# Performance work log

Measured on AMD Instinct MI355X. Metric: run time of the kernel, lower is better.

## Reference

```python
import jax, jax.numpy as jnp
import numpy as np

TRAIN_ROIS = 200
POS_RATIO = 0.33
POS_MAX = int(TRAIN_ROIS * POS_RATIO)  # 66
BBOX_STD = np.array([0.1, 0.1, 0.2, 0.2], dtype=np.float32)


def _iou(boxes1, boxes2):
    # boxes1 [N,4], boxes2 [G,4] in (y1,x1,y2,x2) -> IoU [N,G]
    b1 = boxes1[:, None, :]
    b2 = boxes2[None, :, :]
    y1 = jnp.maximum(b1[..., 0], b2[..., 0])
    x1 = jnp.maximum(b1[..., 1], b2[..., 1])
    y2 = jnp.minimum(b1[..., 2], b2[..., 2])
    x2 = jnp.minimum(b1[..., 3], b2[..., 3])
    inter = jnp.maximum(x2 - x1, 0.0) * jnp.maximum(y2 - y1, 0.0)
    a1 = (b1[..., 2] - b1[..., 0]) * (b1[..., 3] - b1[..., 1])
    a2 = (b2[..., 2] - b2[..., 0]) * (b2[..., 3] - b2[..., 1])
    union = a1 + a2 - inter
    return inter / jnp.where(union > 0, union, 1.0)


def _box_refine(box, gt):
    # standard Mask R-CNN box_refinement_graph
    h = box[..., 2] - box[..., 0]
    w = box[..., 3] - box[..., 1]
    cy = box[..., 0] + 0.5 * h
    cx = box[..., 1] + 0.5 * w
    gh = gt[..., 2] - gt[..., 0]
    gw = gt[..., 3] - gt[..., 1]
    gcy = gt[..., 0] + 0.5 * gh
    gcx = gt[..., 1] + 0.5 * gw
    return jnp.stack([(gcy - cy) / h, (gcx - cx) / w,
                      jnp.log(gh / h), jnp.log(gw / w)], axis=-1)


def _per_image(proposals, gt_boxes, gt_captions, scores):
    T = TRAIN_ROIS
    valid_p = jnp.sum(jnp.abs(proposals), axis=1) > 0   # trim_zeros on proposals
    valid_g = jnp.sum(jnp.abs(gt_boxes), axis=1) > 0    # trim_zeros on gt
    # IoU only feeds comparisons/argmax (pure index selection) -> no grad path
    overlaps = jax.lax.stop_gradient(_iou(proposals, gt_boxes))
    overlaps = jnp.where(valid_g[None, :], overlaps, -1.0)
    roi_iou_max = jnp.max(overlaps, axis=1)
    pos_bool = valid_p & (roi_iou_max >= 0.5)
    neg_bool = valid_p & (roi_iou_max < 0.5)
    # deterministic stand-in for tf.random.shuffle[:count]: first `count` in index order
    pos_idx = jnp.where(pos_bool, size=POS_MAX, fill_value=0)[0]
    pos_cnt = jnp.minimum(jnp.sum(pos_bool), POS_MAX)
    pos_valid = jnp.arange(POS_MAX) < pos_cnt
    neg_target = (pos_cnt.astype(jnp.float32) / POS_RATIO).astype(jnp.int32) - pos_cnt
    neg_idx = jnp.where(neg_bool, size=T, fill_value=0)[0]
    neg_cnt = jnp.minimum(jnp.minimum(neg_target, jnp.sum(neg_bool)), T - pos_cnt)
    neg_valid = jnp.arange(T) < neg_cnt

    positive_rois = proposals[pos_idx]                  # [POS_MAX,4]
    negative_rois = proposals[neg_idx]                  # [T,4]
    gt_assign = jnp.argmax(overlaps[pos_idx], axis=1)   # [POS_MAX]
    roi_gt_boxes = gt_boxes[gt_assign]
    roi_gt_captions = gt_captions[gt_assign]
    roi_gt_scores = scores[gt_assign]
    # for padded (invalid) positive slots, use the roi itself -> zero, finite deltas
    safe_gt = jnp.where(pos_valid[:, None], roi_gt_boxes, positive_rois)
    deltas = _box_refine(positive_rois, safe_gt) / jnp.asarray(BBOX_STD)

    # positives occupy slots [0,pos_cnt), negatives [pos_cnt, pos_cnt+neg_cnt), rest zero-padded
    pos_slots = jnp.where(pos_valid, jnp.arange(POS_MAX), T)   # T is out-of-range -> dropped
    neg_slots = jnp.where(neg_valid, pos_cnt + jnp.arange(T), T)
    rois = (jnp.zeros((T, 4), proposals.dtype)
            .at[pos_slots].set(positive_rois, mode='drop')
            .at[neg_slots].set(negative_rois, mode='drop'))
    out_deltas = jnp.zeros((T, 4), proposals.dtype).at[pos_slots].set(deltas, mode='drop')
    out_caps = jnp.zeros((T, gt_captions.shape[1]), gt_captions.dtype).at[pos_slots].set(roi_gt_captions, mode='drop')
    out_scores = jnp.zeros((T,), scores.dtype).at[pos_slots].set(roi_gt_scores, mode='drop')
    return rois, out_deltas, out_caps, out_scores


def setup_inputs() -> dict:
    key = jax.random.key(0)
    B, N, G = 8, 4096, 512
    k1, k2, k3, k4, k5 = jax.random.split(key, 5)
    c = jax.random.uniform(k1, (B, N, 2))                   # box centers (y,x)
    s = jax.random.uniform(k2, (B, N, 2)) * 0.2 + 0.02      # box sizes
    lo = jnp.clip(c - 0.5 * s, 0.0, 1.0)
    hi = jnp.clip(c + 0.5 * s, 0.0, 1.0)
    proposals = jnp.concatenate([lo, hi], axis=-1)          # (y1,x1,y2,x2)
    # gt boxes = perturbed copies of first G proposals (ensures IoU>=0.5 positives exist)
    p = proposals[:, :G, :] + jax.random.normal(k3, (B, G, 4)) * 0.02
    y1 = jnp.minimum(p[..., 0], p[..., 2]); y2 = jnp.maximum(p[..., 0], p[..., 2]) + 1e-3
    x1 = jnp.minimum(p[..., 1], p[..., 3]); x2 = jnp.maximum(p[..., 1], p[..., 3]) + 1e-3
    gt_boxes = jnp.clip(jnp.stack([y1, x1, y2, x2], axis=-1), 0.0, 1.0)
    # exercise the zero-trim logic: zero-pad tails
    proposals = proposals.at[:, N - 256:, :].set(0.0)
    gt_boxes = gt_boxes.at[:, G - 32:, :].set(0.0)
    gt_captions = jax.random.randint(k4, (B, G, 15), 0, 10000, dtype=jnp.int32)
    scores = jax.random.uniform(k5, (B, G))
    return {"proposals": proposals, "gt_boxes": gt_boxes,
            "gt_captions": gt_captions, "scores": scores}


def reference(proposals, gt_boxes, gt_captions, scores):
    return jax.vmap(_per_image)(proposals, gt_boxes, gt_captions, scores)
```

## Files before the change

### kernel.cpp

```cpp
#include <hip/hip_runtime.h>
#include <math.h>

#define BB   8
#define NP   4096
#define NG   512
#define TT   200
#define PMAX 66

#define CH   8
#define PB   32
#define NBLK (NP / PB)

__global__ __launch_bounds__(256) void iou_phase(
    const float* __restrict__ proposals, const float* __restrict__ gt,
    int* __restrict__ argj, unsigned int* __restrict__ posmask,
    unsigned int* __restrict__ negmask) {
#pragma clang fp contract(off)
  const int b     = blockIdx.x >> 7;
  const int blk   = blockIdx.x & 127;
  const int pbase = blk * PB;

  __shared__ float4 sgt[NG];
  __shared__ float  sa2[NG];
  __shared__ short  sidx[NG];
  __shared__ int    s_nv;
  __shared__ float  rbest[CH][PB];
  __shared__ int    ridx[CH][PB];

  const int tid = threadIdx.x;

  if (tid < 64) {
    const float4* gtb4 = (const float4*)(gt + (size_t)b * NG * 4);
    int cnt = 0;
    for (int base = 0; base < NG; base += 64) {
      int j = base + tid;
      float4 g = gtb4[j];
      bool v = (fabsf(g.x) + fabsf(g.y) + fabsf(g.z) + fabsf(g.w)) > 0.0f;
      unsigned long long m = __ballot(v);
      if (v) {
        int k = cnt + __popcll(m & ((1ull << tid) - 1ull));
        sgt[k]  = g;
        sa2[k]  = (g.z - g.x) * (g.w - g.y);
        sidx[k] = (short)j;
      }
      cnt += __popcll(m);
    }
    if (tid == 0) s_nv = cnt;
  }
  __syncthreads();

  const int nv  = s_nv;
  const int csz = (nv + CH - 1) / CH;

  const int plocal  = tid & (PB - 1);
  const int chunkid = tid >> 5;
  const int i       = pbase + plocal;

  const float4 p = ((const float4*)proposals)[(size_t)b * NP + i];
  const float a1 = (p.z - p.x) * (p.w - p.y);

  int j0 = chunkid * csz;
  int j1 = j0 + csz; if (j1 > nv) j1 = nv;
  if (j0 > nv) j0 = nv;

  float best = -INFINITY;
  int bj = 0;
  for (int j = j0; j < j1; ++j) {
    float4 g = sgt[j];
    float y1 = fmaxf(p.x, g.x);
    float x1 = fmaxf(p.y, g.y);
    float y2 = fminf(p.z, g.z);
    float x2 = fminf(p.w, g.w);
    float inter = fmaxf(x2 - x1, 0.0f) * fmaxf(y2 - y1, 0.0f);
    float un = a1 + sa2[j] - inter;
    float iou = inter / (un > 0.0f ? un : 1.0f);
    if (iou > best) { best = iou; bj = (int)sidx[j]; }
  }
  rbest[chunkid][plocal] = best;
  ridx[chunkid][plocal]  = bj;
  __syncthreads();

  if (tid < PB) {
    float bb = rbest[0][tid];
    int   bi = ridx[0][tid];
    for (int c = 1; c < CH; ++c) {
      float v = rbest[c][tid];
      if (v > bb) { bb = v; bi = ridx[c][tid]; }
    }
    bool vp  = (fabsf(p.x) + fabsf(p.y) + fabsf(p.z) + fabsf(p.w)) > 0.0f;
    bool isp = vp && (bb >= 0.5f);
    bool isn = vp && (bb <  0.5f);
    unsigned long long mp = __ballot(isp);
    unsigned long long mn = __ballot(isn);
    argj[(size_t)b * NP + i] = bi;
    if (tid == 0) {
      posmask[(size_t)b * NBLK + blk] = (unsigned int)mp;
      negmask[(size_t)b * NBLK + blk] = (unsigned int)mn;
    }
  }
}

__global__ __launch_bounds__(256) void select_phase(
    const float* __restrict__ proposals, const float* __restrict__ gt,
    const int* __restrict__ caps, const float* __restrict__ scores,
    const int* __restrict__ argj, const unsigned int* __restrict__ posmask,
    const unsigned int* __restrict__ negmask, float* __restrict__ out) {
#pragma clang fp contract(off)
  const int b = blockIdx.x;

  __shared__ unsigned int s_pm[NBLK], s_nm[NBLK];
  __shared__ int sc[256];
  __shared__ int s_pos[PMAX];
  __shared__ int s_neg[TT];

  const int tid = threadIdx.x;
  const int t   = tid & 127;

  if (tid < NBLK) {
    s_pm[tid] = posmask[(size_t)b * NBLK + tid];
    s_nm[tid] = negmask[(size_t)b * NBLK + tid];
  }
  __syncthreads();

  sc[tid] = (tid < 128) ? __popc(s_pm[t]) : __popc(s_nm[t]);
  __syncthreads();
  for (int off = 1; off < 128; off <<= 1) {
    int v   = sc[tid];
    int add = (t >= off) ? sc[tid - off] : 0;
    __syncthreads();
    sc[tid] = v + add;
    __syncthreads();
  }

  const int pos_total = sc[127];
  const int neg_total = sc[255];

  if (tid < 128) {
    unsigned int pm = s_pm[tid];
    int base = (t == 0) ? 0 : sc[tid - 1];
    while (pm && base < PMAX) {
      int bit = __ffs(pm) - 1;
      s_pos[base] = tid * PB + bit;
      pm &= pm - 1;
      ++base;
    }
  } else {
    unsigned int nm = s_nm[t];
    int base = (t == 0) ? 0 : sc[tid - 1];
    while (nm && base < TT) {
      int bit = __ffs(nm) - 1;
      s_neg[base] = t * PB + bit;
      nm &= nm - 1;
      ++base;
    }
  }
  __syncthreads();

  int pos_cnt = pos_total < PMAX ? pos_total : PMAX;
  int neg_cnt = (int)((float)pos_cnt / 0.33f) - pos_cnt;
  if (neg_total < neg_cnt)    neg_cnt = neg_total;
  if (TT - pos_cnt < neg_cnt) neg_cnt = TT - pos_cnt;
  if (neg_cnt < 0)            neg_cnt = 0;

  float* rois   = out + (size_t)b * TT * 4;
  float* deltas = out + (size_t)BB * TT * 4 + (size_t)b * TT * 4;
  float* ocaps  = out + (size_t)2 * BB * TT * 4 + (size_t)b * TT * 15;
  float* osc    = out + (size_t)2 * BB * TT * 4 + (size_t)BB * TT * 15 + (size_t)b * TT;

  const int k = tid;
  if (k < TT) {
    if (k < pos_cnt) {
      int i = s_pos[k];
      const float* pp = proposals + ((size_t)b * NP + i) * 4;
      float p0 = pp[0], p1 = pp[1], p2 = pp[2], p3 = pp[3];
      int g = argj[(size_t)b * NP + i];
      const float* gg = gt + ((size_t)b * NG + g) * 4;
      float g0 = gg[0], g1 = gg[1], g2 = gg[2], g3 = gg[3];

      rois[k * 4 + 0] = p0; rois[k * 4 + 1] = p1;
      rois[k * 4 + 2] = p2; rois[k * 4 + 3] = p3;

      float h  = p2 - p0, ww = p3 - p1;
      float cy = p0 + 0.5f * h, cx = p1 + 0.5f * ww;
      float gh = g2 - g0, gw = g3 - g1;
      float gcy = g0 + 0.5f * gh, gcx = g1 + 0.5f * gw;
      deltas[k * 4 + 0] = ((gcy - cy) / h) / 0.1f;
      deltas[k * 4 + 1] = ((gcx - cx) / ww) / 0.1f;
      deltas[k * 4 + 2] = logf(gh / h) / 0.2f;
      deltas[k * 4 + 3] = logf(gw / ww) / 0.2f;

      const int* cp = caps + ((size_t)b * NG + g) * 15;
      for (int c = 0; c < 15; ++c) ocaps[k * 15 + c] = (float)cp[c];
      osc[k] = scores[(size_t)b * NG + g];
    } else {
      if (k < pos_cnt + neg_cnt) {
        int i = s_neg[k - pos_cnt];
        const float* pp = proposals + ((size_t)b * NP + i) * 4;
        rois[k * 4 + 0] = pp[0]; rois[k * 4 + 1] = pp[1];
        rois[k * 4 + 2] = pp[2]; rois[k * 4 + 3] = pp[3];
      } else {
        rois[k * 4 + 0] = 0.0f; rois[k * 4 + 1] = 0.0f;
        rois[k * 4 + 2] = 0.0f; rois[k * 4 + 3] = 0.0f;
      }
      deltas[k * 4 + 0] = 0.0f; deltas[k * 4 + 1] = 0.0f;
      deltas[k * 4 + 2] = 0.0f; deltas[k * 4 + 3] = 0.0f;
      for (int c = 0; c < 15; ++c) ocaps[k * 15 + c] = 0.0f;
      osc[k] = 0.0f;
    }
  }
}

extern "C" void kernel_launch(void* const* d_in, const int* in_sizes, int n_in,
                              void* d_out, int out_size, void* d_ws, size_t ws_size,
                              hipStream_t stream) {
  const float* proposals = (const float*)d_in[0];
  const float* gt        = (const float*)d_in[1];
  const int*   caps      = (const int*)d_in[2];
  const float* scores    = (const float*)d_in[3];
  float* out = (float*)d_out;

  char* ws = (char*)d_ws;
  int*          argj = (int*)ws;
  unsigned int* pm   = (unsigned int*)(ws + (size_t)BB * NP * 4);
  unsigned int* nm   = pm + (size_t)BB * NBLK;

  hipLaunchKernelGGL(iou_phase, dim3(BB * NBLK), dim3(256), 0, stream,
                     proposals, gt, argj, pm, nm);
  hipLaunchKernelGGL(select_phase, dim3(BB), dim3(256), 0, stream,
                     proposals, gt, caps, scores, argj, pm, nm, out);
}
```

Before: 81.48 us.

## Parallelize GT compaction across waves and use wave-shuffle scan in selection

The IoU kernel now compacts valid GT boxes with all four waves at once, using per-wave ballot counts and a single shared prefix, instead of one wave looping serially over 512 boxes. The precomputed GT area array is dropped and the area is recomputed in the inner loop. The winning compacted index is mapped back to the original GT index only once per proposal. The selection kernel replaces the block-wide shared-memory Hillis-Steele scan, with its many barriers, by a 64-lane shuffle scan where each lane handles two mask words; this targets barrier and serial latency in tiny, latency-bound kernels, at the cost of a few extra ALU ops per IoU.

```diff
diff --git a/kernel.cpp b/kernel.cpp
--- a/kernel.cpp
+++ b/kernel.cpp
@@ -21,50 +21,56 @@
   const int pbase = blk * PB;
 
   __shared__ float4 sgt[NG];
-  __shared__ float  sa2[NG];
   __shared__ short  sidx[NG];
-  __shared__ int    s_nv;
+  __shared__ int    s_wcnt[4];
   __shared__ float  rbest[CH][PB];
   __shared__ int    ridx[CH][PB];
 
-  const int tid = threadIdx.x;
-
-  if (tid < 64) {
-    const float4* gtb4 = (const float4*)(gt + (size_t)b * NG * 4);
-    int cnt = 0;
-    for (int base = 0; base < NG; base += 64) {
-      int j = base + tid;
-      float4 g = gtb4[j];
-      bool v = (fabsf(g.x) + fabsf(g.y) + fabsf(g.z) + fabsf(g.w)) > 0.0f;
-      unsigned long long m = __ballot(v);
-      if (v) {
-        int k = cnt + __popcll(m & ((1ull << tid) - 1ull));
-        sgt[k]  = g;
-        sa2[k]  = (g.z - g.x) * (g.w - g.y);
-        sidx[k] = (short)j;
-      }
-      cnt += __popcll(m);
-    }
-    if (tid == 0) s_nv = cnt;
-  }
-  __syncthreads();
-
-  const int nv  = s_nv;
-  const int csz = (nv + CH - 1) / CH;
+  const int tid  = threadIdx.x;
+  const int wave = tid >> 6;
+  const int lane = tid & 63;
 
   const int plocal  = tid & (PB - 1);
   const int chunkid = tid >> 5;
   const int i       = pbase + plocal;
 
   const float4 p = ((const float4*)proposals)[(size_t)b * NP + i];
-  const float a1 = (p.z - p.x) * (p.w - p.y);
-
+
+  const float4* gtb4 = (const float4*)(gt + (size_t)b * NG * 4);
+  const int ja = wave * 128 + lane;
+  const int jb = ja + 64;
+  const float4 ga = gtb4[ja];
+  const float4 gb = gtb4[jb];
+  const bool va = (fabsf(ga.x) + fabsf(ga.y) + fabsf(ga.z) + fabsf(ga.w)) > 0.0f;
+  const bool vb = (fabsf(gb.x) + fabsf(gb.y) + fabsf(gb.z) + fabsf(gb.w)) > 0.0f;
+  const unsigned long long ma = __ballot(va);
+  const unsigned long long mb = __ballot(vb);
+  if (lane == 0) s_wcnt[wave] = __popcll(ma) + __popcll(mb);
+  __syncthreads();
+
+  int wbase = 0;
+  for (int w = 0; w < 4; ++w) if (w < wave) wbase += s_wcnt[w];
+  const int nv = s_wcnt[0] + s_wcnt[1] + s_wcnt[2] + s_wcnt[3];
+
+  const unsigned long long lower = (1ull << lane) - 1ull;
+  if (va) {
+    int k = wbase + __popcll(ma & lower);
+    sgt[k] = ga; sidx[k] = (short)ja;
+  }
+  if (vb) {
+    int k = wbase + __popcll(ma) + __popcll(mb & lower);
+    sgt[k] = gb; sidx[k] = (short)jb;
+  }
+  __syncthreads();
+
+  const float a1  = (p.z - p.x) * (p.w - p.y);
+  const int   csz = (nv + CH - 1) / CH;
   int j0 = chunkid * csz;
   int j1 = j0 + csz; if (j1 > nv) j1 = nv;
   if (j0 > nv) j0 = nv;
 
   float best = -INFINITY;
-  int bj = 0;
+  int bk = 0;
   for (int j = j0; j < j1; ++j) {
     float4 g = sgt[j];
     float y1 = fmaxf(p.x, g.x);
@@ -72,12 +78,13 @@
     float y2 = fminf(p.z, g.z);
     float x2 = fminf(p.w, g.w);
     float inter = fmaxf(x2 - x1, 0.0f) * fmaxf(y2 - y1, 0.0f);
-    float un = a1 + sa2[j] - inter;
+    float a2 = (g.z - g.x) * (g.w - g.y);
+    float un = a1 + a2 - inter;
     float iou = inter / (un > 0.0f ? un : 1.0f);
-    if (iou > best) { best = iou; bj = (int)sidx[j]; }
+    if (iou > best) { best = iou; bk = j; }
   }
   rbest[chunkid][plocal] = best;
-  ridx[chunkid][plocal]  = bj;
+  ridx[chunkid][plocal]  = bk;
   __syncthreads();
 
   if (tid < PB) {
@@ -87,12 +94,13 @@
       float v = rbest[c][tid];
       if (v > bb) { bb = v; bi = ridx[c][tid]; }
     }
+    int borig = (int)sidx[bi];
     bool vp  = (fabsf(p.x) + fabsf(p.y) + fabsf(p.z) + fabsf(p.w)) > 0.0f;
     bool isp = vp && (bb >= 0.5f);
     bool isn = vp && (bb <  0.5f);
     unsigned long long mp = __ballot(isp);
     unsigned long long mn = __ballot(isn);
-    argj[(size_t)b * NP + i] = bi;
+    argj[(size_t)b * NP + i] = borig;
     if (tid == 0) {
       posmask[(size_t)b * NBLK + blk] = (unsigned int)mp;
       negmask[(size_t)b * NBLK + blk] = (unsigned int)mn;
@@ -108,54 +116,44 @@
 #pragma clang fp contract(off)
   const int b = blockIdx.x;
 
-  __shared__ unsigned int s_pm[NBLK], s_nm[NBLK];
-  __shared__ int sc[256];
   __shared__ int s_pos[PMAX];
   __shared__ int s_neg[TT];
-
-  const int tid = threadIdx.x;
-  const int t   = tid & 127;
-
-  if (tid < NBLK) {
-    s_pm[tid] = posmask[(size_t)b * NBLK + tid];
-    s_nm[tid] = negmask[(size_t)b * NBLK + tid];
-  }
-  __syncthreads();
-
-  sc[tid] = (tid < 128) ? __popc(s_pm[t]) : __popc(s_nm[t]);
-  __syncthreads();
-  for (int off = 1; off < 128; off <<= 1) {
-    int v   = sc[tid];
-    int add = (t >= off) ? sc[tid - off] : 0;
-    __syncthreads();
-    sc[tid] = v + add;
-    __syncthreads();
-  }
-
-  const int pos_total = sc[127];
-  const int neg_total = sc[255];
-
-  if (tid < 128) {
-    unsigned int pm = s_pm[tid];
-    int base = (t == 0) ? 0 : sc[tid - 1];
-    while (pm && base < PMAX) {
-      int bit = __ffs(pm) - 1;
-      s_pos[base] = tid * PB + bit;
-      pm &= pm - 1;
-      ++base;
-    }
-  } else {
-    unsigned int nm = s_nm[t];
-    int base = (t == 0) ? 0 : sc[tid - 1];
-    while (nm && base < TT) {
-      int bit = __ffs(nm) - 1;
-      s_neg[base] = t * PB + bit;
-      nm &= nm - 1;
-      ++base;
-    }
-  }
-  __syncthreads();
-
+  __shared__ int s_tot[2];
+
+  const int tid  = threadIdx.x;
+  const int wave = tid >> 6;
+  const int lane = tid & 63;
+
+  if (wave < 2) {
+    const unsigned int* msk = (wave == 0 ? posmask : negmask) + (size_t)b * NBLK;
+    const int cap = (wave == 0) ? PMAX : TT;
+    int* list = (wave == 0) ? s_pos : s_neg;
+    unsigned int m0 = msk[2 * lane];
+    unsigned int m1 = msk[2 * lane + 1];
+    int cnt = __popc(m0) + __popc(m1);
+    int incl = cnt;
+    for (int d = 1; d < 64; d <<= 1) {
+      int u = __shfl_up(incl, d, 64);
+      if (lane >= d) incl += u;
+    }
+    int base = incl - cnt;
+    if (lane == 63) s_tot[wave] = incl;
+    while (m0 && base < cap) {
+      int bit = __ffs(m0) - 1;
+      list[base] = lane * 64 + bit;
+      m0 &= m0 - 1; ++base;
+    }
+    int base1 = base + ((base < cap) ? 0 : 0);
+    while (m1 && base1 < cap) {
+      int bit = __ffs(m1) - 1;
+      list[base1] = lane * 64 + 32 + bit;
+      m1 &= m1 - 1; ++base1;
+    }
+  }
+  __syncthreads();
+
+  const int pos_total = s_tot[0];
+  const int neg_total = s_tot[1];
   int pos_cnt = pos_total < PMAX ? pos_total : PMAX;
   int neg_cnt = (int)((float)pos_cnt / 0.33f) - pos_cnt;
   if (neg_total < neg_cnt)    neg_cnt = neg_total;
```

Measured after the change: 80.24 us. Within noise of the previous version (-1.5%).
